# Optimization experiments

Measured on AMD Instinct MI355X. Metric: run time of the kernel, lower is better.

Reference implementation:

```python
import jax, jax.numpy as jnp
import numpy as np

NEG = 1e9  # large negative bias used by the original code for masked positions


def setup_inputs() -> dict:
    key = jax.random.key(0)
    k1, k2, k3 = jax.random.split(key, 3)
    B, H, W, Ck, Cv = 8, 64, 64, 64, 128
    return {
        "query": jax.random.normal(k1, (B, H, W, Ck), dtype=jnp.float32),
        "key": jax.random.normal(k2, (B, H, W, Ck), dtype=jnp.float32),
        "value": jax.random.normal(k3, (B, H, W, Cv), dtype=jnp.float32),
    }


def reference(query, key, value):
    B, Hq, Wq, Ck = query.shape
    Cv = value.shape[-1]
    Nq = Hq * Wq                      # query canvas size
    Nk = key.shape[1] * key.shape[2]  # key/value canvas size

    q = query.reshape(B, Nq, Ck)
    k = key.reshape(B, Nk, Ck)
    v = value.reshape(B, Nk, Cv)

    # strictly-causal pixelSNAIL mask: pixel i may attend only to pixels j < i
    allowed = jnp.tril(jnp.ones((Nq, Nk), dtype=query.dtype), k=-1)

    # [B, Nq, Nk] scaled dot-product scores
    scores = jnp.einsum("bqc,bkc->bqk", q, k) / jnp.sqrt(jnp.asarray(Ck, query.dtype))
    scores = scores - NEG * (1.0 - allowed)

    # softmax then redundant re-mask (as in the original module)
    probs = jax.nn.softmax(scores, axis=-1) * allowed

    out = jnp.einsum("bqk,bkv->bqv", probs, v)
    return out.reshape(B, Hq, Wq, Cv)
```

## Files before the change

### kernel.cpp

```cpp
#include <hip/hip_runtime.h>
#include <hip/hip_bf16.h>

typedef unsigned short u16;
typedef unsigned int u32;
typedef __attribute__((ext_vector_type(2))) unsigned int u32x2;
typedef __attribute__((ext_vector_type(4))) unsigned int u32x4;
typedef __attribute__((ext_vector_type(4))) float f32x4;
typedef __attribute__((ext_vector_type(8))) short bf16x8;
typedef __attribute__((ext_vector_type(16))) float f32x16;

typedef __attribute__((address_space(1))) const void as1_cvoid;
typedef __attribute__((address_space(3))) void as3_void;

__device__ __forceinline__ u32 cvtpk(float lo, float hi) {
    __hip_bfloat162 h = __float22bfloat162_rn(make_float2(lo, hi));
    u32 r; __builtin_memcpy(&r, &h, 4);
    return r;
}
__device__ __forceinline__ int crow(int r, int hl) { return (r & 3) + 8 * (r >> 2) + 4 * hl; }

#define NROW 4096
#define CK 64
#define CV 128
#define TILE_U16 24576
#define WS_NEEDED (8u * 32u * 49152u)
#define SWK(R, o) ((((R) << 7) + (o)) ^ (((R) & 7) << 4))
#define SWVG(R) ((((R) >> 3) & 15) ^ (((R) & 7) << 1))
#define SWV(R, o) ((((R) << 8) + (o)) ^ (SWVG(R) << 4))

__global__ __launch_bounds__(512, 2) void prep_k(const float* __restrict__ Kg,
                                                 const float* __restrict__ Vg,
                                                 u16* __restrict__ ws) {
    int bid = blockIdx.x;
    int b = bid >> 5, jt = bid & 31;
    int t = threadIdx.x;
    int jK = t >> 2, kc4 = t & 3;
    int vg = t & 15, jgrp = t >> 4;
    const float* Kp = Kg + ((size_t)b * NROW + jt * 128) * CK;
    const float* Vp = Vg + ((size_t)b * NROW + jt * 128) * CV;
    u16* img = ws + (size_t)(b * 32 + jt) * TILE_U16;

    {
        const float* kp = Kp + (size_t)jK * CK + kc4 * 16;
        f32x4 a0 = *(const f32x4*)kp,       a1 = *(const f32x4*)(kp + 4);
        f32x4 a2 = *(const f32x4*)(kp + 8), a3 = *(const f32x4*)(kp + 12);
        u32x4 kk0, kk1;
        kk0[0] = cvtpk(a0[0], a0[1]); kk0[1] = cvtpk(a0[2], a0[3]);
        kk0[2] = cvtpk(a1[0], a1[1]); kk0[3] = cvtpk(a1[2], a1[3]);
        kk1[0] = cvtpk(a2[0], a2[1]); kk1[1] = cvtpk(a2[2], a2[3]);
        kk1[2] = cvtpk(a3[0], a3[1]); kk1[3] = cvtpk(a3[2], a3[3]);
        *(u32x4*)&img[SWK(jK, kc4 * 32) >> 1]      = kk0;
        *(u32x4*)&img[SWK(jK, kc4 * 32 + 16) >> 1] = kk1;
    }
    {
        const float* vp = Vp + (size_t)(jgrp * 4) * CV + vg * 8;
        f32x4 va0 = *(const f32x4*)vp,            vb0 = *(const f32x4*)(vp + 4);
        f32x4 va1 = *(const f32x4*)(vp + CV),     vb1 = *(const f32x4*)(vp + CV + 4);
        f32x4 va2 = *(const f32x4*)(vp + 2 * CV), vb2 = *(const f32x4*)(vp + 2 * CV + 4);
        f32x4 va3 = *(const f32x4*)(vp + 3 * CV), vb3 = *(const f32x4*)(vp + 3 * CV + 4);
#pragma unroll
        for (int x = 0; x < 4; x++) {
            u32x2 vv;
            vv[0] = cvtpk(va0[x], va1[x]); vv[1] = cvtpk(va2[x], va3[x]);
            *(u32x2*)&img[8192 + (SWV(vg * 8 + x, jgrp * 8) >> 1)] = vv;
            vv[0] = cvtpk(vb0[x], vb1[x]); vv[1] = cvtpk(vb2[x], vb3[x]);
            *(u32x2*)&img[8192 + (SWV(vg * 8 + 4 + x, jgrp * 8) >> 1)] = vv;
        }
    }
}

__global__ __launch_bounds__(512, 1) void attn_m(const float* __restrict__ Qg,
                                                 const u16* __restrict__ ws,
                                                 float* __restrict__ O) {
    __shared__ __align__(16) u16 smem[2 * TILE_U16 + 16512];

    int bid = blockIdx.x;
    int bb = bid & 7;
    int u  = bid >> 3;
    int t  = threadIdx.x;
    int w  = t >> 6;
    int lane = t & 63;
    int ql = lane & 31, hl = lane >> 5;
    int qsub = w >> 2;
    int jq   = w & 3;
    int uL = u, uH = 63 - u;
    int NR1 = ((2 * uL + 1) >> 2) + 1;
    int NR2 = 33 - NR1;

    const float* Qp = Qg + (size_t)bb * NROW * CK;
    const u16* imgB = ws + (size_t)bb * 32 * TILE_U16;
    const float qscale = 0.125f * 1.44269504088896f;

    bf16x8 qf[4], qfB[4];
    auto loadQ = [&](int T, bf16x8* dst) {
        const float* qb = Qp + (size_t)((T << 5) + ql) * CK;
#pragma unroll
        for (int kc = 0; kc < 4; kc++) {
            const float* qp = qb + kc * 16 + hl * 8;
            f32x4 a = *(const f32x4*)qp;
            f32x4 b2 = *(const f32x4*)(qp + 4);
            u32x4 qq;
            qq[0] = cvtpk(a[0] * qscale, a[1] * qscale);
            qq[1] = cvtpk(a[2] * qscale, a[3] * qscale);
            qq[2] = cvtpk(b2[0] * qscale, b2[1] * qscale);
            qq[3] = cvtpk(b2[2] * qscale, b2[3] * qscale);
            dst[kc] = __builtin_bit_cast(bf16x8, qq);
        }
    };
    int T_cur = 2 * uL + qsub;
    loadQ(T_cur, qf);
    loadQ(2 * uH + qsub, qfB);

    f32x16 acc[4];
#pragma unroll
    for (int vs = 0; vs < 4; vs++)
#pragma unroll
        for (int r = 0; r < 16; r++) acc[vs][r] = 0.f;
    float l = 0.f;

    auto issueTile = [&](int img_tile, int buf_u16) {
        const char* src = (const char*)(imgB + (size_t)img_tile * TILE_U16)
                          + w * 6144 + lane * 16;
        char* dst = (char*)smem + (size_t)buf_u16 * 2 + w * 6144;
#pragma unroll
        for (int i = 0; i < 6; i++)
            __builtin_amdgcn_global_load_lds((as1_cvoid*)(src + i * 1024),
                                             (as3_void*)(dst + i * 1024), 16, 0, 0);
    };

    auto combine = [&](int Tq) {
        float* cm = (float*)&smem[2 * TILE_U16];
        float* lA = cm + 8192;
        float lw = l + __shfl_xor(l, 32);
        if (jq == 0) {
#pragma unroll
            for (int vs = 0; vs < 4; vs++)
#pragma unroll
                for (int r = 0; r < 16; r++)
                    cm[qsub * 4096 + crow(r, hl) * 128 + vs * 32 + ql] = acc[vs][r];
            if (lane < 32) lA[qsub * 32 + lane] = lw;
        }
        __syncthreads();
        if (jq == 1) {
#pragma unroll
            for (int vs = 0; vs < 4; vs++)
#pragma unroll
                for (int r = 0; r < 16; r++)
                    cm[qsub * 4096 + crow(r, hl) * 128 + vs * 32 + ql] += acc[vs][r];
            if (lane < 32) lA[qsub * 32 + lane] += lw;
        }
        __syncthreads();
        if (jq == 2) {
#pragma unroll
            for (int vs = 0; vs < 4; vs++)
#pragma unroll
                for (int r = 0; r < 16; r++)
                    cm[qsub * 4096 + crow(r, hl) * 128 + vs * 32 + ql] += acc[vs][r];
            if (lane < 32) lA[qsub * 32 + lane] += lw;
        }
        __syncthreads();
        if (jq == 3) {
            float ltot = lA[qsub * 32 + ql] + lw;
            float inv = ((Tq << 5) + ql == 0) ? 0.f : 1.f / ltot;
            float inv_r[16];
#pragma unroll
            for (int r = 0; r < 16; r++) inv_r[r] = __shfl(inv, crow(r, hl));
            float* Og = O + ((size_t)bb * NROW + ((size_t)Tq << 5)) * CV;
#pragma unroll
            for (int vs = 0; vs < 4; vs++)
#pragma unroll
                for (int r = 0; r < 16; r++)
                    Og[(size_t)crow(r, hl) * CV + vs * 32 + ql] =
                        (cm[qsub * 4096 + crow(r, hl) * 128 + vs * 32 + ql] + acc[vs][r]) * inv_r[r];
        }
        __syncthreads();
    };

    issueTile(0, 0);

    for (int rr = 0; rr < 33; ++rr) {
        int cur = (rr & 1) * TILE_U16;
        int nxt = ((rr + 1) & 1) * TILE_U16;

        {
            int nr = rr + 1;
            int jb = (nr < NR1) ? nr : (nr - NR1 < NR2 ? nr - NR1 : NR2 - 1);
            issueTile(jb, nxt);
        }
        asm volatile("s_waitcnt vmcnt(6)" ::: "memory");
        __builtin_amdgcn_sched_barrier(0);
        __builtin_amdgcn_s_barrier();

        if (rr == NR1) {
            combine(T_cur);
#pragma unroll
            for (int vs = 0; vs < 4; vs++)
#pragma unroll
                for (int r = 0; r < 16; r++) acc[vs][r] = 0.f;
            l = 0.f;
            T_cur = 2 * uH + qsub;
#pragma unroll
            for (int kc = 0; kc < 4; kc++) qf[kc] = qfB[kc];
        }

        int tt = (rr < NR1) ? rr : rr - NR1;
        int jS = 4 * tt + jq;
        if (jS <= T_cur) {
            __builtin_amdgcn_s_setprio(1);
            bf16x8 kf0 = *(const bf16x8*)&smem[cur + (SWK(jq * 32 + ql, 0 * 32 + hl * 16) >> 1)];
            bf16x8 kf1 = *(const bf16x8*)&smem[cur + (SWK(jq * 32 + ql, 1 * 32 + hl * 16) >> 1)];
            bf16x8 kf2 = *(const bf16x8*)&smem[cur + (SWK(jq * 32 + ql, 2 * 32 + hl * 16) >> 1)];
            bf16x8 kf3 = *(const bf16x8*)&smem[cur + (SWK(jq * 32 + ql, 3 * 32 + hl * 16) >> 1)];
            bf16x8 vf0[4], vf1[4];
#pragma unroll
            for (int vs = 0; vs < 4; vs++) {
                vf0[vs] = *(const bf16x8*)&smem[cur + 8192 + (SWV(vs * 32 + ql, jq * 64 + hl * 16) >> 1)];
                vf1[vs] = *(const bf16x8*)&smem[cur + 8192 + (SWV(vs * 32 + ql, jq * 64 + 32 + hl * 16) >> 1)];
            }

            f32x16 Sa, Sb;
#pragma unroll
            for (int r = 0; r < 16; r++) { Sa[r] = 0.f; Sb[r] = 0.f; }
            Sa = __builtin_amdgcn_mfma_f32_32x32x16_bf16(kf0, qf[0], Sa, 0, 0, 0);
            Sb = __builtin_amdgcn_mfma_f32_32x32x16_bf16(kf2, qf[2], Sb, 0, 0, 0);
            Sa = __builtin_amdgcn_mfma_f32_32x32x16_bf16(kf1, qf[1], Sa, 0, 0, 0);
            Sb = __builtin_amdgcn_mfma_f32_32x32x16_bf16(kf3, qf[3], Sb, 0, 0, 0);

            float P[16];
            bool diag = (jS == T_cur);
#pragma unroll
            for (int r = 0; r < 16; r++) {
                float pr2 = __builtin_exp2f(Sa[r] + Sb[r]);
                if (diag) pr2 = (crow(r, hl) >= ql) ? 0.f : pr2;
                P[r] = pr2;
            }
            {
                float s0 = (P[0] + P[1]) + (P[2] + P[3]);
                float s1 = (P[4] + P[5]) + (P[6] + P[7]);
                float s2 = (P[8] + P[9]) + (P[10] + P[11]);
                float s3 = (P[12] + P[13]) + (P[14] + P[15]);
                l += (s0 + s1) + (s2 + s3);
            }

            u32 A0 = cvtpk(P[0], P[1]),   B0 = cvtpk(P[2], P[3]);
            u32 A1 = cvtpk(P[4], P[5]),   B1 = cvtpk(P[6], P[7]);
            u32 A2 = cvtpk(P[8], P[9]),   B2 = cvtpk(P[10], P[11]);
            u32 A3 = cvtpk(P[12], P[13]), B3 = cvtpk(P[14], P[15]);
            u32 s1 = hl ? A0 : A1, s2 = hl ? B0 : B1;
            u32 s3 = hl ? A2 : A3, s4 = hl ? B2 : B3;
            u32 r1 = (u32)__shfl_xor((int)s1, 32);
            u32 r2 = (u32)__shfl_xor((int)s2, 32);
            u32 r3 = (u32)__shfl_xor((int)s3, 32);
            u32 r4 = (u32)__shfl_xor((int)s4, 32);

            u32x4 w0, w1;
            w0[0] = hl ? r1 : A0; w0[1] = hl ? r2 : B0;
            w0[2] = hl ? A1 : r1; w0[3] = hl ? B1 : r2;
            w1[0] = hl ? r3 : A2; w1[1] = hl ? r4 : B2;
            w1[2] = hl ? A3 : r3; w1[3] = hl ? B3 : r4;
            bf16x8 pa0 = __builtin_bit_cast(bf16x8, w0);
            bf16x8 pa1 = __builtin_bit_cast(bf16x8, w1);

#pragma unroll
            for (int vs = 0; vs < 4; vs++)
                acc[vs] = __builtin_amdgcn_mfma_f32_32x32x16_bf16(pa0, vf0[vs], acc[vs], 0, 0, 0);
#pragma unroll
            for (int vs = 0; vs < 4; vs++)
                acc[vs] = __builtin_amdgcn_mfma_f32_32x32x16_bf16(pa1, vf1[vs], acc[vs], 0, 0, 0);
            __builtin_amdgcn_s_setprio(0);
        }
        __builtin_amdgcn_s_barrier();
    }

    combine(T_cur);
}

#define FBUF 24576
#define FVT 8192
__global__ __launch_bounds__(512, 2) void attn_fb(const float* __restrict__ Qg,
                                                  const float* __restrict__ Kg,
                                                  const float* __restrict__ Vg,
                                                  float* __restrict__ O) {
    __shared__ __align__(16) u16 smem[2 * FBUF];
    int bid = blockIdx.x;
    int bb = bid & 7;
    int u  = bid >> 3;
    int t  = threadIdx.x;
    int w  = t >> 6;
    int lane = t & 63;
    int ql = lane & 31, hl = lane >> 5;
    int qsub = w >> 2, jq = w & 3;
    int uL = u, uH = 63 - u;
    int rA = ((2 * uL + 1) >> 2) + 1;
    const float* Qp = Qg + (size_t)bb * NROW * CK;
    const float* Kp = Kg + (size_t)bb * NROW * CK;
    const float* Vp = Vg + (size_t)bb * NROW * CV;
    const float qscale = 0.125f * 1.44269504088896f;
    bf16x8 qf[4];
    auto loadQ = [&](int T) {
        const float* qb = Qp + (size_t)((T << 5) + ql) * CK;
#pragma unroll
        for (int kc = 0; kc < 4; kc++) {
            const float* qp = qb + kc * 16 + hl * 8;
            f32x4 a = *(const f32x4*)qp;
            f32x4 b2 = *(const f32x4*)(qp + 4);
            u32x4 qq;
            qq[0] = cvtpk(a[0] * qscale, a[1] * qscale);
            qq[1] = cvtpk(a[2] * qscale, a[3] * qscale);
            qq[2] = cvtpk(b2[0] * qscale, b2[1] * qscale);
            qq[3] = cvtpk(b2[2] * qscale, b2[3] * qscale);
            qf[kc] = __builtin_bit_cast(bf16x8, qq);
        }
    };
    int T_cur = 2 * uL + qsub;
    loadQ(T_cur);
    f32x16 acc[4];
#pragma unroll
    for (int vs = 0; vs < 4; vs++)
#pragma unroll
        for (int r = 0; r < 16; r++) acc[vs][r] = 0.f;
    float l = 0.f;
    int jK = t >> 2, kc4 = t & 3;
    int vg = t & 15, jgrp = t >> 4;
    const float* kSrc = Kp + (size_t)jK * CK + kc4 * 16;
    const float* vSrc = Vp + (size_t)(jgrp * 4) * CV + vg * 8;
    f32x4 kr0, kr1, kr2, kr3, va0, va1, va2, va3, vb0, vb1, vb2, vb3;
    auto prefetch = [&](int jb) {
        const float* kp = kSrc + (size_t)jb * CK;
        kr0 = *(const f32x4*)kp;       kr1 = *(const f32x4*)(kp + 4);
        kr2 = *(const f32x4*)(kp + 8); kr3 = *(const f32x4*)(kp + 12);
        const float* vp = vSrc + (size_t)jb * CV;
        va0 = *(const f32x4*)vp;            vb0 = *(const f32x4*)(vp + 4);
        va1 = *(const f32x4*)(vp + CV);     vb1 = *(const f32x4*)(vp + CV + 4);
        va2 = *(const f32x4*)(vp + 2 * CV); vb2 = *(const f32x4*)(vp + 2 * CV + 4);
        va3 = *(const f32x4*)(vp + 3 * CV); vb3 = *(const f32x4*)(vp + 3 * CV + 4);
    };
    auto store_tile = [&](int bufo) {
        u32x4 kk0, kk1;
        kk0[0] = cvtpk(kr0[0], kr0[1]); kk0[1] = cvtpk(kr0[2], kr0[3]);
        kk0[2] = cvtpk(kr1[0], kr1[1]); kk0[3] = cvtpk(kr1[2], kr1[3]);
        kk1[0] = cvtpk(kr2[0], kr2[1]); kk1[1] = cvtpk(kr2[2], kr2[3]);
        kk1[2] = cvtpk(kr3[0], kr3[1]); kk1[3] = cvtpk(kr3[2], kr3[3]);
        *(u32x4*)&smem[bufo + (SWK(jK, kc4 * 32) >> 1)]      = kk0;
        *(u32x4*)&smem[bufo + (SWK(jK, kc4 * 32 + 16) >> 1)] = kk1;
#pragma unroll
        for (int x = 0; x < 4; x++) {
            int v = vg * 8 + x;
            u32x2 vv; vv[0] = cvtpk(va0[x], va1[x]); vv[1] = cvtpk(va2[x], va3[x]);
            *(u32x2*)&smem[bufo + FVT + (SWV(v, jgrp * 8) >> 1)] = vv;
        }
#pragma unroll
        for (int x = 0; x < 4; x++) {
            int v = vg * 8 + 4 + x;
            u32x2 vv; vv[0] = cvtpk(vb0[x], vb1[x]); vv[1] = cvtpk(vb2[x], vb3[x]);
            *(u32x2*)&smem[bufo + FVT + (SWV(v, jgrp * 8) >> 1)] = vv;
        }
    };
    auto combine = [&](int scratch, int Tq) {
        float* cm = (float*)(smem + scratch);
        float* lA = cm + 8192;
        float lw = l + __shfl_xor(l, 32);
        if (jq == 0) {
#pragma unroll
            for (int vs = 0; vs < 4; vs++)
#pragma unroll
                for (int r = 0; r < 16; r++)
                    cm[qsub * 4096 + crow(r, hl) * 128 + vs * 32 + ql] = acc[vs][r];
            if (lane < 32) lA[qsub * 32 + lane] = lw;
        }
        __syncthreads();
        if (jq == 1) {
#pragma unroll
            for (int vs = 0; vs < 4; vs++)
#pragma unroll
                for (int r = 0; r < 16; r++)
                    cm[qsub * 4096 + crow(r, hl) * 128 + vs * 32 + ql] += acc[vs][r];
            if (lane < 32) lA[qsub * 32 + lane] += lw;
        }
        __syncthreads();
        if (jq == 2) {
#pragma unroll
            for (int vs = 0; vs < 4; vs++)
#pragma unroll
                for (int r = 0; r < 16; r++)
                    cm[qsub * 4096 + crow(r, hl) * 128 + vs * 32 + ql] += acc[vs][r];
            if (lane < 32) lA[qsub * 32 + lane] += lw;
        }
        __syncthreads();
        if (jq == 3) {
            float ltot = lA[qsub * 32 + ql] + lw;
            float inv = ((Tq << 5) + ql == 0) ? 0.f : 1.f / ltot;
            float inv_r[16];
#pragma unroll
            for (int r = 0; r < 16; r++) inv_r[r] = __shfl(inv, crow(r, hl));
            float* Og = O + ((size_t)bb * NROW + ((size_t)Tq << 5)) * CV;
#pragma unroll
            for (int vs = 0; vs < 4; vs++)
#pragma unroll
                for (int r = 0; r < 16; r++)
                    Og[(size_t)crow(r, hl) * CV + vs * 32 + ql] =
                        (cm[qsub * 4096 + crow(r, hl) * 128 + vs * 32 + ql] + acc[vs][r]) * inv_r[r];
        }
        __syncthreads();
    };
    prefetch(0);
    for (int rr = 0; rr < 33; ++rr) {
        int bufo = (rr & 1) * FBUF;
        store_tile(bufo);
        __syncthreads();
        if (rr == rA) {
            combine(((rA - 1) & 1) * FBUF, T_cur);
#pragma unroll
            for (int vs = 0; vs < 4; vs++)
#pragma unroll
                for (int r = 0; r < 16; r++) acc[vs][r] = 0.f;
            l = 0.f;
            T_cur = 2 * uH + qsub;
            loadQ(T_cur);
        }
        int tt = (rr < rA) ? rr : rr - rA;
        int jS = 4 * tt + jq;
        {
            int nr = rr + 1;
            int jb = (nr < rA) ? (nr << 7)
                               : ((nr <= 32 ? (nr - rA) : (32 - rA)) << 7);
            prefetch(jb);
        }
        if (jS > T_cur) continue;
        bf16x8 kf0 = *(const bf16x8*)&smem[bufo + (SWK(jq * 32 + ql, 0 * 32 + hl * 16) >> 1)];
        bf16x8 kf1 = *(const bf16x8*)&smem[bufo + (SWK(jq * 32 + ql, 1 * 32 + hl * 16) >> 1)];
        bf16x8 kf2 = *(const bf16x8*)&smem[bufo + (SWK(jq * 32 + ql, 2 * 32 + hl * 16) >> 1)];
        bf16x8 kf3 = *(const bf16x8*)&smem[bufo + (SWK(jq * 32 + ql, 3 * 32 + hl * 16) >> 1)];
        f32x16 S;
#pragma unroll
        for (int r = 0; r < 16; r++) S[r] = 0.f;
        __builtin_amdgcn_s_setprio(1);
        S = __builtin_amdgcn_mfma_f32_32x32x16_bf16(kf0, qf[0], S, 0, 0, 0);
        S = __builtin_amdgcn_mfma_f32_32x32x16_bf16(kf1, qf[1], S, 0, 0, 0);
        S = __builtin_amdgcn_mfma_f32_32x32x16_bf16(kf2, qf[2], S, 0, 0, 0);
        S = __builtin_amdgcn_mfma_f32_32x32x16_bf16(kf3, qf[3], S, 0, 0, 0);
        __builtin_amdgcn_s_setprio(0);
        float P[16];
        bool diag = (jS == T_cur);
#pragma unroll
        for (int r = 0; r < 16; r++) {
            float pr2 = __builtin_exp2f(S[r]);
            if (diag) pr2 = (crow(r, hl) >= ql) ? 0.f : pr2;
            P[r] = pr2;
        }
        {
            float s0 = (P[0] + P[1]) + (P[2] + P[3]);
            float s1 = (P[4] + P[5]) + (P[6] + P[7]);
            float s2 = (P[8] + P[9]) + (P[10] + P[11]);
            float s3 = (P[12] + P[13]) + (P[14] + P[15]);
            l += (s0 + s1) + (s2 + s3);
        }
        u32 A0 = cvtpk(P[0], P[1]),   B0 = cvtpk(P[2], P[3]);
        u32 A1 = cvtpk(P[4], P[5]),   B1 = cvtpk(P[6], P[7]);
        u32 A2 = cvtpk(P[8], P[9]),   B2 = cvtpk(P[10], P[11]);
        u32 A3 = cvtpk(P[12], P[13]), B3 = cvtpk(P[14], P[15]);
        u32 s1 = hl ? A0 : A1, s2 = hl ? B0 : B1;
        u32 s3 = hl ? A2 : A3, s4 = hl ? B2 : B3;
        u32 r1 = (u32)__shfl_xor((int)s1, 32);
        u32 r2 = (u32)__shfl_xor((int)s2, 32);
        u32 r3 = (u32)__shfl_xor((int)s3, 32);
        u32 r4 = (u32)__shfl_xor((int)s4, 32);
        bf16x8 vf0[4], vf1[4];
#pragma unroll
        for (int vs = 0; vs < 4; vs++) {
            vf0[vs] = *(const bf16x8*)&smem[bufo + FVT + (SWV(vs * 32 + ql, jq * 64 + hl * 16) >> 1)];
            vf1[vs] = *(const bf16x8*)&smem[bufo + FVT + (SWV(vs * 32 + ql, jq * 64 + 32 + hl * 16) >> 1)];
        }
        u32x4 w0, w1;
        w0[0] = hl ? r1 : A0; w0[1] = hl ? r2 : B0;
        w0[2] = hl ? A1 : r1; w0[3] = hl ? B1 : r2;
        w1[0] = hl ? r3 : A2; w1[1] = hl ? r4 : B2;
        w1[2] = hl ? A3 : r3; w1[3] = hl ? B3 : r4;
        bf16x8 pa0 = __builtin_bit_cast(bf16x8, w0);
        bf16x8 pa1 = __builtin_bit_cast(bf16x8, w1);
        __builtin_amdgcn_s_setprio(1);
#pragma unroll
        for (int vs = 0; vs < 4; vs++)
            acc[vs] = __builtin_amdgcn_mfma_f32_32x32x16_bf16(pa0, vf0[vs], acc[vs], 0, 0, 0);
#pragma unroll
        for (int vs = 0; vs < 4; vs++)
            acc[vs] = __builtin_amdgcn_mfma_f32_32x32x16_bf16(pa1, vf1[vs], acc[vs], 0, 0, 0);
        __builtin_amdgcn_s_setprio(0);
    }
    __syncthreads();
    combine(0, T_cur);
}

extern "C" void kernel_launch(void* const* d_in, const int* in_sizes, int n_in,
                              void* d_out, int out_size, void* d_ws, size_t ws_size,
                              hipStream_t stream) {
    const float* Q = (const float*)d_in[0];
    const float* K = (const float*)d_in[1];
    const float* V = (const float*)d_in[2];
    float* out = (float*)d_out;
    if (ws_size >= (size_t)WS_NEEDED) {
        u16* ws = (u16*)d_ws;
        hipLaunchKernelGGL(prep_k, dim3(256), dim3(512), 0, stream, K, V, ws);
        hipLaunchKernelGGL(attn_m, dim3(256), dim3(512), 0, stream, Q, ws, out);
    } else {
        hipLaunchKernelGGL(attn_fb, dim3(256), dim3(512), 0, stream, Q, K, V, out);
    }
}
```

Baseline: 77.95 us.

## Read bf16 K and transposed V directly from global instead of LDS staging

```diff
diff --git a/kernel.cpp b/kernel.cpp
--- a/kernel.cpp
+++ b/kernel.cpp
@@ -3,15 +3,11 @@
 
 typedef unsigned short u16;
 typedef unsigned int u32;
-typedef __attribute__((ext_vector_type(2))) unsigned int u32x2;
 typedef __attribute__((ext_vector_type(4))) unsigned int u32x4;
 typedef __attribute__((ext_vector_type(4))) float f32x4;
 typedef __attribute__((ext_vector_type(8))) short bf16x8;
 typedef __attribute__((ext_vector_type(16))) float f32x16;
 
-typedef __attribute__((address_space(1))) const void as1_cvoid;
-typedef __attribute__((address_space(3))) void as3_void;
-
 __device__ __forceinline__ u32 cvtpk(float lo, float hi) {
     __hip_bfloat162 h = __float22bfloat162_rn(make_float2(lo, hi));
     u32 r; __builtin_memcpy(&r, &h, 4);
@@ -22,57 +18,48 @@
 #define NROW 4096
 #define CK 64
 #define CV 128
-#define TILE_U16 24576
-#define WS_NEEDED (8u * 32u * 49152u)
-#define SWK(R, o) ((((R) << 7) + (o)) ^ (((R) & 7) << 4))
-#define SWVG(R) ((((R) >> 3) & 15) ^ (((R) & 7) << 1))
-#define SWV(R, o) ((((R) << 8) + (o)) ^ (SWVG(R) << 4))
-
-__global__ __launch_bounds__(512, 2) void prep_k(const float* __restrict__ Kg,
-                                                 const float* __restrict__ Vg,
-                                                 u16* __restrict__ ws) {
-    int bid = blockIdx.x;
-    int b = bid >> 5, jt = bid & 31;
+#define KB_U16 (8u * 4096u * 64u)
+#define WS_NEEDED (4194304u + 8388608u)
+
+__global__ __launch_bounds__(256, 4) void prep_kb(const float* __restrict__ Kg,
+                                                  u16* __restrict__ Kb) {
+    int i = blockIdx.x * 256 + threadIdx.x;
+    const f32x4* p = (const f32x4*)Kg + (size_t)i * 2;
+    f32x4 a = p[0], b = p[1];
+    u32x4 r;
+    r[0] = cvtpk(a[0], a[1]); r[1] = cvtpk(a[2], a[3]);
+    r[2] = cvtpk(b[0], b[1]); r[3] = cvtpk(b[2], b[3]);
+    *((u32x4*)Kb + i) = r;
+}
+
+__global__ __launch_bounds__(256, 2) void prep_vt(const float* __restrict__ Vg,
+                                                  u16* __restrict__ Vt) {
+    __shared__ u16 lds[64][65];
+    int blk = blockIdx.x;
+    int ct = blk & 1, rt = (blk >> 1) & 63, b = blk >> 7;
+    const float* src = Vg + ((size_t)b * NROW + (size_t)rt * 64) * CV + (size_t)ct * 64;
+    u16* dst = Vt + ((size_t)b * CV + (size_t)ct * 64) * NROW + (size_t)rt * 64;
     int t = threadIdx.x;
-    int jK = t >> 2, kc4 = t & 3;
-    int vg = t & 15, jgrp = t >> 4;
-    const float* Kp = Kg + ((size_t)b * NROW + jt * 128) * CK;
-    const float* Vp = Vg + ((size_t)b * NROW + jt * 128) * CV;
-    u16* img = ws + (size_t)(b * 32 + jt) * TILE_U16;
-
-    {
-        const float* kp = Kp + (size_t)jK * CK + kc4 * 16;
-        f32x4 a0 = *(const f32x4*)kp,       a1 = *(const f32x4*)(kp + 4);
-        f32x4 a2 = *(const f32x4*)(kp + 8), a3 = *(const f32x4*)(kp + 12);
-        u32x4 kk0, kk1;
-        kk0[0] = cvtpk(a0[0], a0[1]); kk0[1] = cvtpk(a0[2], a0[3]);
-        kk0[2] = cvtpk(a1[0], a1[1]); kk0[3] = cvtpk(a1[2], a1[3]);
-        kk1[0] = cvtpk(a2[0], a2[1]); kk1[1] = cvtpk(a2[2], a2[3]);
-        kk1[2] = cvtpk(a3[0], a3[1]); kk1[3] = cvtpk(a3[2], a3[3]);
-        *(u32x4*)&img[SWK(jK, kc4 * 32) >> 1]      = kk0;
-        *(u32x4*)&img[SWK(jK, kc4 * 32 + 16) >> 1] = kk1;
+#pragma unroll
+    for (int i = 0; i < 16; i++) {
+        int li = i * 256 + t; int r = li >> 6, c = li & 63;
+        __hip_bfloat16 h = __float2bfloat16(src[(size_t)r * CV + c]);
+        u16 v; __builtin_memcpy(&v, &h, 2);
+        lds[r][c] = v;
     }
-    {
-        const float* vp = Vp + (size_t)(jgrp * 4) * CV + vg * 8;
-        f32x4 va0 = *(const f32x4*)vp,            vb0 = *(const f32x4*)(vp + 4);
-        f32x4 va1 = *(const f32x4*)(vp + CV),     vb1 = *(const f32x4*)(vp + CV + 4);
-        f32x4 va2 = *(const f32x4*)(vp + 2 * CV), vb2 = *(const f32x4*)(vp + 2 * CV + 4);
-        f32x4 va3 = *(const f32x4*)(vp + 3 * CV), vb3 = *(const f32x4*)(vp + 3 * CV + 4);
-#pragma unroll
-        for (int x = 0; x < 4; x++) {
-            u32x2 vv;
-            vv[0] = cvtpk(va0[x], va1[x]); vv[1] = cvtpk(va2[x], va3[x]);
-            *(u32x2*)&img[8192 + (SWV(vg * 8 + x, jgrp * 8) >> 1)] = vv;
-            vv[0] = cvtpk(vb0[x], vb1[x]); vv[1] = cvtpk(vb2[x], vb3[x]);
-            *(u32x2*)&img[8192 + (SWV(vg * 8 + 4 + x, jgrp * 8) >> 1)] = vv;
-        }
+    __syncthreads();
+#pragma unroll
+    for (int i = 0; i < 16; i++) {
+        int li = i * 256 + t; int c = li >> 6, r = li & 63;
+        dst[(size_t)c * NROW + r] = lds[r][c];
     }
 }
 
 __global__ __launch_bounds__(512, 1) void attn_m(const float* __restrict__ Qg,
-                                                 const u16* __restrict__ ws,
+                                                 const u16* __restrict__ Kb,
+                                                 const u16* __restrict__ Vt,
                                                  float* __restrict__ O) {
-    __shared__ __align__(16) u16 smem[2 * TILE_U16 + 16512];
+    __shared__ __align__(16) u16 smem[16512];
 
     int bid = blockIdx.x;
     int bb = bid & 7;
@@ -83,12 +70,10 @@
     int ql = lane & 31, hl = lane >> 5;
     int qsub = w >> 2;
     int jq   = w & 3;
-    int uL = u, uH = 63 - u;
-    int NR1 = ((2 * uL + 1) >> 2) + 1;
-    int NR2 = 33 - NR1;
 
     const float* Qp = Qg + (size_t)bb * NROW * CK;
-    const u16* imgB = ws + (size_t)bb * 32 * TILE_U16;
+    const u16* Kp = Kb + (size_t)bb * NROW * CK;
+    const u16* Vp = Vt + (size_t)bb * CV * NROW;
     const float qscale = 0.125f * 1.44269504088896f;
 
     bf16x8 qf[4], qfB[4];
@@ -107,9 +92,9 @@
             dst[kc] = __builtin_bit_cast(bf16x8, qq);
         }
     };
-    int T_cur = 2 * uL + qsub;
-    loadQ(T_cur, qf);
-    loadQ(2 * uH + qsub, qfB);
+    int T_A = 2 * u + qsub, T_B = 2 * (63 - u) + qsub;
+    loadQ(T_A, qf);
+    loadQ(T_B, qfB);
 
     f32x16 acc[4];
 #pragma unroll
@@ -118,18 +103,11 @@
         for (int r = 0; r < 16; r++) acc[vs][r] = 0.f;
     float l = 0.f;
 
-    auto issueTile = [&](int img_tile, int buf_u16) {
-        const char* src = (const char*)(imgB + (size_t)img_tile * TILE_U16)
-                          + w * 6144 + lane * 16;
-        char* dst = (char*)smem + (size_t)buf_u16 * 2 + w * 6144;
-#pragma unroll
-        for (int i = 0; i < 6; i++)
-            __builtin_amdgcn_global_load_lds((as1_cvoid*)(src + i * 1024),
-                                             (as3_void*)(dst + i * 1024), 16, 0, 0);
-    };
+    const u16* kLane = Kp + (size_t)ql * CK + hl * 8;
+    const u16* vLane0 = Vp + (size_t)ql * NROW + hl * 8;
 
     auto combine = [&](int Tq) {
-        float* cm = (float*)&smem[2 * TILE_U16];
+        float* cm = (float*)smem;
         float* lA = cm + 8192;
         float lw = l + __shfl_xor(l, 32);
         if (jq == 0) {
@@ -176,51 +154,33 @@
         __syncthreads();
     };
 
-    issueTile(0, 0);
-
-    for (int rr = 0; rr < 33; ++rr) {
-        int cur = (rr & 1) * TILE_U16;
-        int nxt = ((rr + 1) & 1) * TILE_U16;
-
-        {
-            int nr = rr + 1;
-            int jb = (nr < NR1) ? nr : (nr - NR1 < NR2 ? nr - NR1 : NR2 - 1);
-            issueTile(jb, nxt);
-        }
-        asm volatile("s_waitcnt vmcnt(6)" ::: "memory");
-        __builtin_amdgcn_sched_barrier(0);
-        __builtin_amdgcn_s_barrier();
-
-        if (rr == NR1) {
-            combine(T_cur);
-#pragma unroll
-            for (int vs = 0; vs < 4; vs++)
-#pragma unroll
-                for (int r = 0; r < 16; r++) acc[vs][r] = 0.f;
-            l = 0.f;
-            T_cur = 2 * uH + qsub;
+#pragma unroll 1
+    for (int phase = 0; phase < 2; ++phase) {
+        int T_cur = phase ? T_B : T_A;
+        if (phase) {
 #pragma unroll
             for (int kc = 0; kc < 4; kc++) qf[kc] = qfB[kc];
         }
 
-        int tt = (rr < NR1) ? rr : rr - NR1;
-        int jS = 4 * tt + jq;
-        if (jS <= T_cur) {
+#pragma unroll 1
+        for (int jS = jq; jS <= T_cur; jS += 4) {
+            const u16* kp = kLane + (size_t)jS * 2048;
+            bf16x8 kf0 = *(const bf16x8*)(kp);
+            bf16x8 kf1 = *(const bf16x8*)(kp + 16);
+            bf16x8 kf2 = *(const bf16x8*)(kp + 32);
+            bf16x8 kf3 = *(const bf16x8*)(kp + 48);
+            const u16* vp = vLane0 + (size_t)jS * 32;
+            bf16x8 vf0[4], vf1[4];
+#pragma unroll
+            for (int vs = 0; vs < 4; vs++) {
+                vf0[vs] = *(const bf16x8*)(vp + (size_t)vs * 32 * NROW);
+                vf1[vs] = *(const bf16x8*)(vp + (size_t)vs * 32 * NROW + 16);
+            }
+
+            f32x16 Sa, Sb;
+#pragma unroll
+            for (int r = 0; r < 16; r++) { Sa[r] = 0.f; Sb[r] = 0.f; }
             __builtin_amdgcn_s_setprio(1);
-            bf16x8 kf0 = *(const bf16x8*)&smem[cur + (SWK(jq * 32 + ql, 0 * 32 + hl * 16) >> 1)];
-            bf16x8 kf1 = *(const bf16x8*)&smem[cur + (SWK(jq * 32 + ql, 1 * 32 + hl * 16) >> 1)];
-            bf16x8 kf2 = *(const bf16x8*)&smem[cur + (SWK(jq * 32 + ql, 2 * 32 + hl * 16) >> 1)];
-            bf16x8 kf3 = *(const bf16x8*)&smem[cur + (SWK(jq * 32 + ql, 3 * 32 + hl * 16) >> 1)];
-            bf16x8 vf0[4], vf1[4];
-#pragma unroll
-            for (int vs = 0; vs < 4; vs++) {
-                vf0[vs] = *(const bf16x8*)&smem[cur + 8192 + (SWV(vs * 32 + ql, jq * 64 + hl * 16) >> 1)];
-                vf1[vs] = *(const bf16x8*)&smem[cur + 8192 + (SWV(vs * 32 + ql, jq * 64 + 32 + hl * 16) >> 1)];
-            }
-
-            f32x16 Sa, Sb;
-#pragma unroll
-            for (int r = 0; r < 16; r++) { Sa[r] = 0.f; Sb[r] = 0.f; }
             Sa = __builtin_amdgcn_mfma_f32_32x32x16_bf16(kf0, qf[0], Sa, 0, 0, 0);
             Sb = __builtin_amdgcn_mfma_f32_32x32x16_bf16(kf2, qf[2], Sb, 0, 0, 0);
             Sa = __builtin_amdgcn_mfma_f32_32x32x16_bf16(kf1, qf[1], Sa, 0, 0, 0);
@@ -269,14 +229,24 @@
                 acc[vs] = __builtin_amdgcn_mfma_f32_32x32x16_bf16(pa1, vf1[vs], acc[vs], 0, 0, 0);
             __builtin_amdgcn_s_setprio(0);
         }
-        __builtin_amdgcn_s_barrier();
+
+        combine(T_cur);
+        if (!phase) {
+#pragma unroll
+            for (int vs = 0; vs < 4; vs++)
+#pragma unroll
+                for (int r = 0; r < 16; r++) acc[vs][r] = 0.f;
+            l = 0.f;
+        }
     }
-
-    combine(T_cur);
-}
-
+}
+
+typedef __attribute__((ext_vector_type(2))) unsigned int u32x2;
 #define FBUF 24576
 #define FVT 8192
+#define SWK(R, o) ((((R) << 7) + (o)) ^ (((R) & 7) << 4))
+#define SWVG(R) ((((R) >> 3) & 15) ^ (((R) & 7) << 1))
+#define FSWV(R, o) ((((R) << 8) + (o)) ^ (SWVG(R) << 4))
 __global__ __launch_bounds__(512, 2) void attn_fb(const float* __restrict__ Qg,
                                                   const float* __restrict__ Kg,
                                                   const float* __restrict__ Vg,
@@ -347,13 +317,13 @@
         for (int x = 0; x < 4; x++) {
             int v = vg * 8 + x;
             u32x2 vv; vv[0] = cvtpk(va0[x], va1[x]); vv[1] = cvtpk(va2[x], va3[x]);
-            *(u32x2*)&smem[bufo + FVT + (SWV(v, jgrp * 8) >> 1)] = vv;
+            *(u32x2*)&smem[bufo + FVT + (FSWV(v, jgrp * 8) >> 1)] = vv;
         }
 #pragma unroll
         for (int x = 0; x < 4; x++) {
             int v = vg * 8 + 4 + x;
             u32x2 vv; vv[0] = cvtpk(vb0[x], vb1[x]); vv[1] = cvtpk(vb2[x], vb3[x]);
-            *(u32x2*)&smem[bufo + FVT + (SWV(v, jgrp * 8) >> 1)] = vv;
+            *(u32x2*)&smem[bufo + FVT + (FSWV(v, jgrp * 8) >> 1)] = vv;
         }
     };
     auto combine = [&](int scratch, int Tq) {
@@ -468,8 +438,8 @@
         bf16x8 vf0[4], vf1[4];
 #pragma unroll
         for (int vs = 0; vs < 4; vs++) {
-            vf0[vs] = *(const bf16x8*)&smem[bufo + FVT + (SWV(vs * 32 + ql, jq * 64 + hl * 16) >> 1)];
-            vf1[vs] = *(const bf16x8*)&smem[bufo + FVT + (SWV(vs * 32 + ql, jq * 64 + 32 + hl * 16) >> 1)];
+            vf0[vs] = *(const bf16x8*)&smem[bufo + FVT + (FSWV(vs * 32 + ql, jq * 64 + hl * 16) >> 1)];
+            vf1[vs] = *(const bf16x8*)&smem[bufo + FVT + (FSWV(vs * 32 + ql, jq * 64 + 32 + hl * 16) >> 1)];
         }
         u32x4 w0, w1;
         w0[0] = hl ? r1 : A0; w0[1] = hl ? r2 : B0;
@@ -499,9 +469,11 @@
     const float* V = (const float*)d_in[2];
     float* out = (float*)d_out;
     if (ws_size >= (size_t)WS_NEEDED) {
-        u16* ws = (u16*)d_ws;
-        hipLaunchKernelGGL(prep_k, dim3(256), dim3(512), 0, stream, K, V, ws);
-        hipLaunchKernelGGL(attn_m, dim3(256), dim3(512), 0, stream, Q, ws, out);
+        u16* Kb = (u16*)d_ws;
+        u16* Vt = Kb + KB_U16;
+        hipLaunchKernelGGL(prep_kb, dim3(1024), dim3(256), 0, stream, K, Kb);
+        hipLaunchKernelGGL(prep_vt, dim3(1024), dim3(256), 0, stream, V, Vt);
+        hipLaunchKernelGGL(attn_m, dim3(256), dim3(512), 0, stream, Q, Kb, Vt, out);
     } else {
         hipLaunchKernelGGL(attn_fb, dim3(256), dim3(512), 0, stream, Q, K, V, out);
     }
```

Result: slower. 115.7 us (+48.5%).
